# Kernel optimization log

Measured on AMD Instinct MI355X. Metric: run time of the kernel, lower is better.

## Reference

```python
import jax, jax.numpy as jnp
import numpy as np
from jax import lax

B, L = 16, 2048
D_TOK, D_TIS = 256, 64
D_MODEL = D_TOK + D_TIS          # 320
EXPAND = 2
D_INNER = EXPAND * D_MODEL       # 640
D_STATE = 16
D_CONV = 4
DT_RANK = (D_MODEL + 15) // 16   # 20 (ceil(d_model/16), Mamba default)
H_OUT = 128
VOCAB = 65                       # len(CODON_MAP_DNA)+1
N_TISSUES = 30
MAX_NORM = 2.0


def _embed_maxnorm(W, idx):
    # torch nn.Embedding(max_norm=2): looked-up rows are renormalized to norm<=2
    e = W[idx]
    n = jnp.linalg.norm(e, axis=-1, keepdims=True)
    return e * jnp.minimum(1.0, MAX_NORM / jnp.maximum(n, 1e-12))


def setup_inputs() -> dict:
    key = jax.random.key(0)
    ks = jax.random.split(key, 18)
    s = 0.02
    seq_W = jax.random.normal(ks[3], (VOCAB, D_TOK), dtype=jnp.float32)
    seq_W = seq_W.at[0].set(0.0)  # padding_idx=0
    A_log = jnp.log(jnp.broadcast_to(jnp.arange(1, D_STATE + 1, dtype=jnp.float32), (D_INNER, D_STATE)))
    return {
        "rna_data_pad": jax.random.randint(ks[0], (B, L), 0, VOCAB).astype(jnp.int32),
        "tissue_id": jax.random.randint(ks[1], (B,), 0, N_TISSUES).astype(jnp.int32),
        "seq_lengths": jax.random.randint(ks[2], (B,), 1, L + 1).astype(jnp.int32),
        "seq_W": seq_W,
        "tissue_W": jax.random.normal(ks[4], (N_TISSUES, D_TIS), dtype=jnp.float32),
        "in_proj_W": jax.random.normal(ks[5], (2 * D_INNER, D_MODEL), dtype=jnp.float32) * s,
        "conv_w": jax.random.normal(ks[6], (D_INNER, 1, D_CONV), dtype=jnp.float32) * s,
        "conv_b": jnp.zeros((D_INNER,), dtype=jnp.float32),
        "x_proj_W": jax.random.normal(ks[7], (DT_RANK + 2 * D_STATE, D_INNER), dtype=jnp.float32) * s,
        "dt_proj_W": jax.random.normal(ks[8], (D_INNER, DT_RANK), dtype=jnp.float32) * s,
        "dt_proj_b": jax.random.uniform(ks[9], (D_INNER,), minval=-4.0, maxval=-2.0),
        "A_log": A_log,
        "D_skip": jnp.ones((D_INNER,), dtype=jnp.float32),
        "out_proj_W": jax.random.normal(ks[10], (D_MODEL, D_INNER), dtype=jnp.float32) * s,
        "p1_W": jax.random.normal(ks[11], (H_OUT, D_MODEL), dtype=jnp.float32) * s,
        "p1_b": jnp.zeros((H_OUT,), dtype=jnp.float32),
        "p2_W": jax.random.normal(ks[12], (1, H_OUT), dtype=jnp.float32) * s,
        "p2_b": jnp.zeros((1,), dtype=jnp.float32),
    }


def reference(rna_data_pad, tissue_id, seq_lengths, seq_W, tissue_W, in_proj_W,
              conv_w, conv_b, x_proj_W, dt_proj_W, dt_proj_b, A_log, D_skip,
              out_proj_W, p1_W, p1_b, p2_W, p2_b):
    b, l = rna_data_pad.shape
    # embeddings + tissue broadcast + mask
    seq_emb = _embed_maxnorm(seq_W, rna_data_pad)            # [B,L,D_TOK]
    tis_emb = _embed_maxnorm(tissue_W, tissue_id)            # [B,D_TIS]
    tis_exp = jnp.broadcast_to(tis_emb[:, None, :], (b, l, tis_emb.shape[-1]))
    x = jnp.concatenate([seq_emb, tis_exp], axis=-1)          # [B,L,D_MODEL]
    x = x * (rna_data_pad != 0)[..., None]
    # Mamba block
    xz = x @ in_proj_W.T                                      # [B,L,2*D_INNER]
    xm, z = jnp.split(xz, 2, axis=-1)
    xt = xm.transpose(0, 2, 1)                                # [B,D_INNER,L]
    conv = lax.conv_general_dilated(
        xt, conv_w, window_strides=(1,), padding=[(D_CONV - 1, 0)],
        feature_group_count=D_INNER,
        dimension_numbers=("NCH", "OIH", "NCH")) + conv_b[None, :, None]
    xm = jax.nn.silu(conv).transpose(0, 2, 1)                 # [B,L,D_INNER]
    x_dbl = xm @ x_proj_W.T                                   # [B,L,DT_RANK+2*D_STATE]
    dt, Bm, Cm = jnp.split(x_dbl, [DT_RANK, DT_RANK + D_STATE], axis=-1)
    delta = jax.nn.softplus(dt @ dt_proj_W.T + dt_proj_b)     # [B,L,D_INNER]
    A = -jnp.exp(A_log)                                       # [D_INNER,D_STATE]
    # selective scan over time
    xs = (delta.transpose(1, 0, 2), Bm.transpose(1, 0, 2),
          Cm.transpose(1, 0, 2), xm.transpose(1, 0, 2))
    h0 = jnp.zeros((b, D_INNER, D_STATE), dtype=xm.dtype)

    def step(h, t):
        dl, bt, ct, ut = t                                    # [B,di],[B,ds],[B,ds],[B,di]
        dA = jnp.exp(dl[:, :, None] * A)                      # [B,di,ds]
        dBu = (dl * ut)[:, :, None] * bt[:, None, :]          # [B,di,ds]
        h = dA * h + dBu
        y = jnp.einsum("bds,bs->bd", h, ct)
        return h, y

    _, ys = lax.scan(step, h0, xs)                            # ys: [L,B,D_INNER]
    y = ys.transpose(1, 0, 2) + xm * D_skip
    y = y * jax.nn.silu(z)
    out = y @ out_proj_W.T                                    # [B,L,D_MODEL]
    # gather last valid timestep
    out_last = out[jnp.arange(b), seq_lengths - 1]            # [B,D_MODEL]
    h1 = jax.nn.relu(out_last @ p1_W.T + p1_b)
    return h1 @ p2_W.T + p2_b                                 # [B,1]
```

## Files before the change

### kernel.cpp

```cpp
#include <hip/hip_runtime.h>
#include <hip/hip_bf16.h>
#include <math.h>

#define B_      16
#define L_      2048
#define D_MODEL 320
#define D_INNER 640
#define D_STATE 16
#define DT_RANK 20
#define H_OUT   128
#define VOCAB   65
#define N_TIS   30
#define TT      8
#define ST      64
#define NCHUNK  16
#define CHLEN   (L_/NCHUNK)

static constexpr size_t OFF_MSEQ  = 0;
static constexpr size_t OFF_MTIS  = OFF_MSEQ + VOCAB*1280;
static constexpr size_t OFF_YSCAN = OFF_MTIS + N_TIS*1280;
static constexpr size_t OFF_CLAST = OFF_YSCAN + B_*D_INNER;
static constexpr size_t OFF_XD    = OFF_CLAST + B_*16;
static constexpr size_t OFF_PC    = OFF_XD + (size_t)B_*L_*36;
static constexpr size_t OFF_SC    = OFF_PC + (size_t)B_*NCHUNK*40*256;

__device__ __forceinline__ float silu_f(float x) { return x / (1.0f + __expf(-x)); }

__global__ __launch_bounds__(256) void k_mbuild(
    const float* __restrict__ seqW, const float* __restrict__ tisW,
    const float* __restrict__ inW, float* __restrict__ ws)
{
    __shared__ float a_l[256];
    __shared__ float red[4];
    int v = blockIdx.x, tid = threadIdx.x;
    int K, wofs; const float* src; float* dstM;
    if (v < VOCAB) { K = 256; wofs = 0;   src = seqW + (size_t)v*256;        dstM = ws + OFF_MSEQ + (size_t)v*1280; }
    else           { K = 64;  wofs = 256; src = tisW + (size_t)(v-VOCAB)*64; dstM = ws + OFF_MTIS + (size_t)(v-VOCAB)*1280; }
    float x = (tid < K) ? src[tid] : 0.0f;
    float ss = x * x;
    #pragma unroll
    for (int o = 32; o; o >>= 1) ss += __shfl_xor(ss, o);
    if ((tid & 63) == 0) red[tid >> 6] = ss;
    __syncthreads();
    float tot = red[0] + red[1] + red[2] + red[3];
    float scale = fminf(1.0f, 2.0f / fmaxf(sqrtf(tot), 1e-12f));
    if (tid < K) a_l[tid] = x * scale;
    __syncthreads();

    int j = blockIdx.y * 256 + tid;
    const float* w = inW + (size_t)j*320 + wofs;
    float ac0 = 0.f, ac1 = 0.f, ac2 = 0.f, ac3 = 0.f;
    #pragma unroll 4
    for (int k = 0; k < K; k += 4) {
        float4 w4 = *(const float4*)(w + k);
        ac0 += a_l[k+0]*w4.x; ac1 += a_l[k+1]*w4.y;
        ac2 += a_l[k+2]*w4.z; ac3 += a_l[k+3]*w4.w;
    }
    dstM[j] = (ac0 + ac1) + (ac2 + ac3);
}

__global__ __launch_bounds__(256) void k_xdbl(
    const int* __restrict__ idx, const int* __restrict__ tissue_id,
    const int* __restrict__ seq_lengths,
    const float* __restrict__ conv_w, const float* __restrict__ conv_b,
    const float* __restrict__ xW, float* __restrict__ ws)
{
    __shared__ float u_l[TT*641];
    __shared__ float xd_l[TT*36];
    __shared__ int   idx_l[TT+3];
    int b = blockIdx.y;
    int t0 = blockIdx.x * TT;
    int t_last = seq_lengths[b] - 1;
    if (t0 > t_last) return;
    int tid = threadIdx.x;
    const float* Mseq = ws + OFF_MSEQ;
    const float* Mtis = ws + OFF_MTIS;
    int tis = tissue_id[b];
    if (tid < TT+3) {
        int t = t0 - 3 + tid;
        idx_l[tid] = (t >= 0) ? idx[b*L_ + t] : 0;
    }
    __syncthreads();

    for (int d = tid; d < D_INNER; d += 256) {
        float w0 = conv_w[d*4+0], w1 = conv_w[d*4+1], w2 = conv_w[d*4+2], w3 = conv_w[d*4+3];
        float cb = conv_b[d];
        float mt = Mtis[(size_t)tis*1280 + d];
        auto XZ = [&](int k) -> float {
            int row = idx_l[k];
            return row ? (Mseq[(size_t)row*1280 + d] + mt) : 0.0f;
        };
        float a0 = XZ(0), a1 = XZ(1), a2 = XZ(2);
        for (int t = 0; t < TT; ++t) {
            float a3 = XZ(t+3);
            float c = w0*a0 + w1*a1 + w2*a2 + w3*a3 + cb;
            u_l[t*641 + d] = silu_f(c);
            a0 = a1; a1 = a2; a2 = a3;
        }
    }
    __syncthreads();

    {
        int w = tid >> 6, l = tid & 63;
        float wreg[9][10];
        #pragma unroll
        for (int kk = 0; kk < 9; ++kk) {
            const float* xr = xW + (size_t)(w + 4*kk)*D_INNER + l;
            #pragma unroll
            for (int i = 0; i < 10; ++i) wreg[kk][i] = xr[64*i];
        }
        for (int t = 0; t < TT; ++t) {
            float p[9];
            #pragma unroll
            for (int kk = 0; kk < 9; ++kk) p[kk] = 0.f;
            #pragma unroll
            for (int i = 0; i < 10; ++i) {
                float ui = u_l[t*641 + l + 64*i];
                #pragma unroll
                for (int kk = 0; kk < 9; ++kk) p[kk] = fmaf(wreg[kk][i], ui, p[kk]);
            }
            #pragma unroll
            for (int o = 32; o; o >>= 1) {
                #pragma unroll
                for (int kk = 0; kk < 9; ++kk) p[kk] += __shfl_xor(p[kk], o);
            }
            if (l == t) {
                #pragma unroll
                for (int kk = 0; kk < 9; ++kk) xd_l[t*36 + w + 4*kk] = p[kk];
            }
        }
        if (t_last < t0 + TT) {
            int tl = t_last - t0;
            float pc[4];
            #pragma unroll
            for (int k = 0; k < 4; ++k) pc[k] = 0.f;
            #pragma unroll
            for (int i = 0; i < 10; ++i) {
                float ui = u_l[tl*641 + l + 64*i];
                #pragma unroll
                for (int k = 0; k < 4; ++k)
                    pc[k] = fmaf(xW[(size_t)(36 + w + 4*k)*D_INNER + l + 64*i], ui, pc[k]);
            }
            #pragma unroll
            for (int o = 32; o; o >>= 1) {
                #pragma unroll
                for (int k = 0; k < 4; ++k) pc[k] += __shfl_xor(pc[k], o);
            }
            if (l == 0) {
                #pragma unroll
                for (int k = 0; k < 4; ++k) ws[OFF_CLAST + b*16 + w + 4*k] = pc[k];
            }
        }
    }
    __syncthreads();

    {
        int tmax = min(TT-1, t_last - t0);
        int cnt = (tmax + 1) * 36;
        float* dst = ws + OFF_XD + ((size_t)b*L_ + t0)*36;
        for (int o = tid; o < cnt; o += 256) dst[o] = xd_l[o];
    }
}

__global__ __launch_bounds__(256) void k_scanc(
    const int* __restrict__ idx, const int* __restrict__ tissue_id,
    const int* __restrict__ seq_lengths,
    const float* __restrict__ conv_w, const float* __restrict__ conv_b,
    const float* __restrict__ dtW, const float* __restrict__ dtb,
    const float* __restrict__ A_log, float* __restrict__ ws)
{
    __shared__ float xd_t[ST*36];
    __shared__ float dl_t[16*72];
    __shared__ float du_t[16*72];
    __shared__ int   idx_t[ST+3];

    int b = blockIdx.y, dg = blockIdx.x, c = blockIdx.z;
    int t_last = seq_lengths[b] - 1;
    int t_begin = c * CHLEN;
    if (t_begin > t_last) return;
    int t_end = min(t_begin + CHLEN - 1, t_last);
    int tid = threadIdx.x;
    int dl = tid >> 4, s = tid & 15;
    int dd = tid & 15, tg = tid >> 4;
    int d_own = dg*16 + dd;
    int tis = tissue_id[b];
    const float* Mseq = ws + OFF_MSEQ;

    float dtw_r[20];
    #pragma unroll
    for (int i = 0; i < 20; i += 4) {
        float4 w4 = *(const float4*)(dtW + d_own*20 + i);
        dtw_r[i] = w4.x; dtw_r[i+1] = w4.y; dtw_r[i+2] = w4.z; dtw_r[i+3] = w4.w;
    }
    float4 cw4 = *(const float4*)(conv_w + d_own*4);
    float  cb  = conv_b[d_own];
    float  dtb_v = dtb[d_own];
    float  mt  = ws[OFF_MTIS + (size_t)tis*1280 + d_own];
    float As = -__expf(A_log[(dg*16 + dl)*D_STATE + s]) * 1.44269504089f;

    float h = 0.0f;
    float sd = 0.0f;
    for (int t0 = t_begin; t0 <= t_end; t0 += ST) {
        int nt = min(ST, t_end - t0 + 1);
        if (tid < ST+3) {
            int t = t0 - 3 + tid;
            idx_t[tid] = (t >= 0 && t < L_) ? idx[b*L_ + t] : 0;
        }
        {
            const float4* src = (const float4*)(ws + OFF_XD + ((size_t)b*L_ + t0)*36);
            float4* dst = (float4*)xd_t;
            int cnt4 = nt * 9;
            for (int o = tid; o < cnt4; o += 256) dst[o] = src[o];
        }
        __syncthreads();

        {
            int ttb = tg * 4;
            if (ttb < nt) {
                float xz[7];
                #pragma unroll
                for (int k = 0; k < 7; ++k) {
                    int row = idx_t[ttb + k];
                    xz[k] = row ? (Mseq[(size_t)row*1280 + d_own] + mt) : 0.0f;
                }
                float dl4[4], du4[4];
                bool full = (ttb + 3 < nt);
                #pragma unroll
                for (int j = 0; j < 4; ++j) {
                    int tt = ttb + j;
                    if (full || tt < nt) {
                        float cc = cb;
                        cc = fmaf(cw4.x, xz[j+0], cc);
                        cc = fmaf(cw4.y, xz[j+1], cc);
                        cc = fmaf(cw4.z, xz[j+2], cc);
                        cc = fmaf(cw4.w, xz[j+3], cc);
                        float u = silu_f(cc);
                        const float* xr = xd_t + tt*36;
                        float x = dtb_v;
                        #pragma unroll
                        for (int r = 0; r < 20; r += 4) {
                            float4 x4 = *(const float4*)(xr + r);
                            x = fmaf(x4.x, dtw_r[r+0], x);
                            x = fmaf(x4.y, dtw_r[r+1], x);
                            x = fmaf(x4.z, dtw_r[r+2], x);
                            x = fmaf(x4.w, dtw_r[r+3], x);
                        }
                        float e = __expf(-fabsf(x));
                        float sp = fmaxf(x, 0.0f) + __logf(1.0f + e);
                        dl4[j] = sp;
                        du4[j] = sp * u;
                    } else { dl4[j] = 0.f; du4[j] = 0.f; }
                }
                if (full) {
                    *(float4*)(dl_t + dd*72 + ttb) = make_float4(dl4[0], dl4[1], dl4[2], dl4[3]);
                    *(float4*)(du_t + dd*72 + ttb) = make_float4(du4[0], du4[1], du4[2], du4[3]);
                } else {
                    for (int j = 0; j < 4 && ttb + j < nt; ++j) {
                        dl_t[dd*72 + ttb + j] = dl4[j];
                        du_t[dd*72 + ttb + j] = du4[j];
                    }
                }
            }
        }
        __syncthreads();

        {
            int q4 = nt >> 2;
            for (int q = 0; q < q4; ++q) {
                float4 d4 = *(const float4*)(dl_t + dl*72 + 4*q);
                float4 u4 = *(const float4*)(du_t + dl*72 + 4*q);
                float b0 = xd_t[(4*q+0)*36 + 20 + s];
                float b1 = xd_t[(4*q+1)*36 + 20 + s];
                float b2 = xd_t[(4*q+2)*36 + 20 + s];
                float b3 = xd_t[(4*q+3)*36 + 20 + s];
                h = fmaf(exp2f(d4.x*As), h, u4.x*b0);
                h = fmaf(exp2f(d4.y*As), h, u4.y*b1);
                h = fmaf(exp2f(d4.z*As), h, u4.z*b2);
                h = fmaf(exp2f(d4.w*As), h, u4.w*b3);
                sd += (d4.x + d4.y) + (d4.z + d4.w);
            }
            for (int tt = q4*4; tt < nt; ++tt) {
                float dlt = dl_t[dl*72 + tt];
                h = fmaf(exp2f(dlt * As), h, du_t[dl*72 + tt] * xd_t[tt*36 + 20 + s]);
                sd += dlt;
            }
        }
        __syncthreads();
    }
    float P = exp2f(As * sd);
    size_t base = (((size_t)b*NCHUNK + c)*40 + dg)*256 + tid;
    ws[OFF_PC + base] = P;
    ws[OFF_SC + base] = h;
}

__global__ __launch_bounds__(320) void k_final(
    const int* __restrict__ idx, const int* __restrict__ tissue_id,
    const int* __restrict__ seq_lengths,
    const float* __restrict__ conv_w, const float* __restrict__ conv_b,
    const float* __restrict__ Dskip, const float* __restrict__ outW,
    const float* __restrict__ p1W, const float* __restrict__ p1b,
    const float* __restrict__ p2W, const float* __restrict__ p2b,
    const float* __restrict__ ws, float* __restrict__ out)
{
    __shared__ float y_l[D_INNER];
    __shared__ float o_l[D_MODEL];
    __shared__ float h1_l[H_OUT];
    __shared__ float cl_l[16];
    int b = blockIdx.x, tid = threadIdx.x;
    int t_last = seq_lengths[b] - 1;
    int ncv = t_last / CHLEN + 1;
    int tis = tissue_id[b];
    const float* Mseq = ws + OFF_MSEQ;
    const float* Mtis = ws + OFF_MTIS;
    if (tid < 16) cl_l[tid] = ws[OFF_CLAST + b*16 + tid];
    __syncthreads();

    int rows[4];
    #pragma unroll
    for (int k = 0; k < 4; ++k) {
        int t = t_last - 3 + k;
        rows[k] = (t >= 0) ? idx[b*L_ + t] : 0;
    }
    for (int d = tid; d < D_INNER; d += 320) {
        int dgg = d >> 4, dll = d & 15;
        float hs[16];
        #pragma unroll
        for (int s = 0; s < 16; ++s) hs[s] = 0.0f;
        for (int c = 0; c < ncv; ++c) {
            const float* pc = ws + OFF_PC + (((size_t)b*NCHUNK + c)*40 + dgg)*256 + dll*16;
            const float* sc = ws + OFF_SC + (((size_t)b*NCHUNK + c)*40 + dgg)*256 + dll*16;
            #pragma unroll
            for (int s4 = 0; s4 < 4; ++s4) {
                float4 p = *(const float4*)(pc + 4*s4);
                float4 sv = *(const float4*)(sc + 4*s4);
                hs[4*s4+0] = fmaf(p.x, hs[4*s4+0], sv.x);
                hs[4*s4+1] = fmaf(p.y, hs[4*s4+1], sv.y);
                hs[4*s4+2] = fmaf(p.z, hs[4*s4+2], sv.z);
                hs[4*s4+3] = fmaf(p.w, hs[4*s4+3], sv.w);
            }
        }
        float ys = 0.0f;
        #pragma unroll
        for (int s = 0; s < 16; ++s) ys = fmaf(hs[s], cl_l[s], ys);

        float conv = conv_b[d];
        const float* cw = conv_w + d*4;
        #pragma unroll
        for (int k = 0; k < 4; ++k) {
            int row = rows[k];
            float xzv = row ? (Mseq[(size_t)row*1280 + d] + Mtis[(size_t)tis*1280 + d]) : 0.0f;
            conv += cw[k] * xzv;
        }
        float u = silu_f(conv);
        int rowL = rows[3];
        float z = rowL ? (Mseq[(size_t)rowL*1280 + 640 + d] + Mtis[(size_t)tis*1280 + 640 + d]) : 0.0f;
        y_l[d] = (ys + u * Dskip[d]) * silu_f(z);
    }
    __syncthreads();
    if (tid < D_MODEL) {
        const float* w = outW + tid*D_INNER;
        float acc = 0.f;
        #pragma unroll 4
        for (int k = 0; k < D_INNER; k += 4) {
            float4 w4 = *(const float4*)(w + k);
            acc += y_l[k]*w4.x + y_l[k+1]*w4.y + y_l[k+2]*w4.z + y_l[k+3]*w4.w;
        }
        o_l[tid] = acc;
    }
    __syncthreads();
    if (tid < H_OUT) {
        const float* w = p1W + tid*D_MODEL;
        float acc = p1b[tid];
        #pragma unroll 4
        for (int k = 0; k < D_MODEL; k += 4) {
            float4 w4 = *(const float4*)(w + k);
            acc += o_l[k]*w4.x + o_l[k+1]*w4.y + o_l[k+2]*w4.z + o_l[k+3]*w4.w;
        }
        h1_l[tid] = fmaxf(acc, 0.0f);
    }
    __syncthreads();
    if (tid == 0) {
        float acc = p2b[0];
        for (int k = 0; k < H_OUT; ++k) acc += h1_l[k]*p2W[k];
        out[b] = acc;
    }
}

extern "C" void kernel_launch(void* const* d_in, const int* in_sizes, int n_in,
                              void* d_out, int out_size, void* d_ws, size_t ws_size,
                              hipStream_t stream)
{
    const int*   idx   = (const int*)d_in[0];
    const int*   tis   = (const int*)d_in[1];
    const int*   slen  = (const int*)d_in[2];
    const float* seqW  = (const float*)d_in[3];
    const float* tisW  = (const float*)d_in[4];
    const float* inW   = (const float*)d_in[5];
    const float* convw = (const float*)d_in[6];
    const float* convb = (const float*)d_in[7];
    const float* xW    = (const float*)d_in[8];
    const float* dtW   = (const float*)d_in[9];
    const float* dtb   = (const float*)d_in[10];
    const float* Alog  = (const float*)d_in[11];
    const float* Dsk   = (const float*)d_in[12];
    const float* outW  = (const float*)d_in[13];
    const float* p1W   = (const float*)d_in[14];
    const float* p1b   = (const float*)d_in[15];
    const float* p2W   = (const float*)d_in[16];
    const float* p2b   = (const float*)d_in[17];
    float* ws  = (float*)d_ws;
    float* out = (float*)d_out;

    hipLaunchKernelGGL(k_mbuild, dim3(VOCAB + N_TIS, 5), dim3(256), 0, stream, seqW, tisW, inW, ws);
    hipLaunchKernelGGL(k_xdbl,   dim3(L_/TT, B_),        dim3(256), 0, stream,
                       idx, tis, slen, convw, convb, xW, ws);
    hipLaunchKernelGGL(k_scanc,  dim3(D_INNER/16, B_, NCHUNK), dim3(256), 0, stream,
                       idx, tis, slen, convw, convb, dtW, dtb, Alog, ws);
    hipLaunchKernelGGL(k_final,  dim3(B_),               dim3(320), 0, stream,
                       idx, tis, slen, convw, convb, Dsk, outW, p1W, p1b, p2W, p2b, ws, out);
}
```

Measured before the change: 276.1 us.

## Split chunk-state combine into a parallel kernel and preload conv inputs

Moves the cross-chunk state recurrence and C-projection out of the 16-block k_final into a new k_comb kernel with 640 blocks. Each thread there handles one (d, s) pair and reduces over s with warp shuffles, then writes y_scan to workspace for k_final to read. This is meant to remove the serial, low-parallelism combine that ran inside k_final. It also preloads the TT+3 conv inputs into registers in k_xdbl and unrolls the conv with fmaf, at the cost of one extra kernel launch.

```diff
diff --git a/kernel.cpp b/kernel.cpp
--- a/kernel.cpp
+++ b/kernel.cpp
@@ -86,16 +86,20 @@
         float w0 = conv_w[d*4+0], w1 = conv_w[d*4+1], w2 = conv_w[d*4+2], w3 = conv_w[d*4+3];
         float cb = conv_b[d];
         float mt = Mtis[(size_t)tis*1280 + d];
-        auto XZ = [&](int k) -> float {
+        float xzv[TT+3];
+        #pragma unroll
+        for (int k = 0; k < TT+3; ++k) {
             int row = idx_l[k];
-            return row ? (Mseq[(size_t)row*1280 + d] + mt) : 0.0f;
-        };
-        float a0 = XZ(0), a1 = XZ(1), a2 = XZ(2);
+            xzv[k] = row ? (Mseq[(size_t)row*1280 + d] + mt) : 0.0f;
+        }
+        #pragma unroll
         for (int t = 0; t < TT; ++t) {
-            float a3 = XZ(t+3);
-            float c = w0*a0 + w1*a1 + w2*a2 + w3*a3 + cb;
+            float c = cb;
+            c = fmaf(w0, xzv[t+0], c);
+            c = fmaf(w1, xzv[t+1], c);
+            c = fmaf(w2, xzv[t+2], c);
+            c = fmaf(w3, xzv[t+3], c);
             u_l[t*641 + d] = silu_f(c);
-            a0 = a1; a1 = a2; a2 = a3;
         }
     }
     __syncthreads();
@@ -293,6 +297,25 @@
     ws[OFF_SC + base] = h;
 }
 
+__global__ __launch_bounds__(256) void k_comb(const int* __restrict__ seq_lengths,
+                                              float* __restrict__ ws)
+{
+    int b = blockIdx.y, dg = blockIdx.x;
+    int tid = threadIdx.x;
+    int dl = tid >> 4, s = tid & 15;
+    int t_last = seq_lengths[b] - 1;
+    int ncv = t_last / CHLEN + 1;
+    float h = 0.0f;
+    for (int c = 0; c < ncv; ++c) {
+        size_t base = (((size_t)b*NCHUNK + c)*40 + dg)*256 + tid;
+        h = fmaf(ws[OFF_PC + base], h, ws[OFF_SC + base]);
+    }
+    float v = h * ws[OFF_CLAST + b*16 + s];
+    v += __shfl_xor(v, 1); v += __shfl_xor(v, 2);
+    v += __shfl_xor(v, 4); v += __shfl_xor(v, 8);
+    if (s == 0) ws[OFF_YSCAN + (size_t)b*D_INNER + dg*16 + dl] = v;
+}
+
 __global__ __launch_bounds__(320) void k_final(
     const int* __restrict__ idx, const int* __restrict__ tissue_id,
     const int* __restrict__ seq_lengths,
@@ -305,16 +328,11 @@
     __shared__ float y_l[D_INNER];
     __shared__ float o_l[D_MODEL];
     __shared__ float h1_l[H_OUT];
-    __shared__ float cl_l[16];
     int b = blockIdx.x, tid = threadIdx.x;
     int t_last = seq_lengths[b] - 1;
-    int ncv = t_last / CHLEN + 1;
     int tis = tissue_id[b];
     const float* Mseq = ws + OFF_MSEQ;
     const float* Mtis = ws + OFF_MTIS;
-    if (tid < 16) cl_l[tid] = ws[OFF_CLAST + b*16 + tid];
-    __syncthreads();
-
     int rows[4];
     #pragma unroll
     for (int k = 0; k < 4; ++k) {
@@ -322,27 +340,6 @@
         rows[k] = (t >= 0) ? idx[b*L_ + t] : 0;
     }
     for (int d = tid; d < D_INNER; d += 320) {
-        int dgg = d >> 4, dll = d & 15;
-        float hs[16];
-        #pragma unroll
-        for (int s = 0; s < 16; ++s) hs[s] = 0.0f;
-        for (int c = 0; c < ncv; ++c) {
-            const float* pc = ws + OFF_PC + (((size_t)b*NCHUNK + c)*40 + dgg)*256 + dll*16;
-            const float* sc = ws + OFF_SC + (((size_t)b*NCHUNK + c)*40 + dgg)*256 + dll*16;
-            #pragma unroll
-            for (int s4 = 0; s4 < 4; ++s4) {
-                float4 p = *(const float4*)(pc + 4*s4);
-                float4 sv = *(const float4*)(sc + 4*s4);
-                hs[4*s4+0] = fmaf(p.x, hs[4*s4+0], sv.x);
-                hs[4*s4+1] = fmaf(p.y, hs[4*s4+1], sv.y);
-                hs[4*s4+2] = fmaf(p.z, hs[4*s4+2], sv.z);
-                hs[4*s4+3] = fmaf(p.w, hs[4*s4+3], sv.w);
-            }
-        }
-        float ys = 0.0f;
-        #pragma unroll
-        for (int s = 0; s < 16; ++s) ys = fmaf(hs[s], cl_l[s], ys);
-
         float conv = conv_b[d];
         const float* cw = conv_w + d*4;
         #pragma unroll
@@ -354,6 +351,7 @@
         float u = silu_f(conv);
         int rowL = rows[3];
         float z = rowL ? (Mseq[(size_t)rowL*1280 + 640 + d] + Mtis[(size_t)tis*1280 + 640 + d]) : 0.0f;
+        float ys = ws[OFF_YSCAN + (size_t)b*D_INNER + d];
         y_l[d] = (ys + u * Dskip[d]) * silu_f(z);
     }
     __syncthreads();
@@ -416,6 +414,7 @@
                        idx, tis, slen, convw, convb, xW, ws);
     hipLaunchKernelGGL(k_scanc,  dim3(D_INNER/16, B_, NCHUNK), dim3(256), 0, stream,
                        idx, tis, slen, convw, convb, dtW, dtb, Alog, ws);
+    hipLaunchKernelGGL(k_comb,   dim3(D_INNER/16, B_),   dim3(256), 0, stream, slen, ws);
     hipLaunchKernelGGL(k_final,  dim3(B_),               dim3(320), 0, stream,
                        idx, tis, slen, convw, convb, Dsk, outW, p1W, p1b, p2W, p2b, ws, out);
 }
```

Result: no change. 271.8 us (-1.5%).
